# Optimization experiments

Measured on AMD Instinct MI355X. Metric: run time of the kernel, lower is better.

Reference implementation:

```python
import jax, jax.numpy as jnp
import numpy as np

EMBD_SIZE = 128
NUM_HEADS = 8
HEAD_SIZE = 16

def setup_inputs() -> dict:
    key = jax.random.key(0)
    ks = jax.random.split(key, 6)
    B, S = 8, 2048
    x = jax.random.normal(ks[0], (B, S, EMBD_SIZE), dtype=jnp.float32)
    # per-head Linear weights, torch layout [out, in] stacked over heads -> [H, hs, E]
    sc = 1.0 / np.sqrt(EMBD_SIZE)
    Wk = jax.random.normal(ks[1], (NUM_HEADS, HEAD_SIZE, EMBD_SIZE), dtype=jnp.float32) * sc
    Wq = jax.random.normal(ks[2], (NUM_HEADS, HEAD_SIZE, EMBD_SIZE), dtype=jnp.float32) * sc
    Wv = jax.random.normal(ks[3], (NUM_HEADS, HEAD_SIZE, EMBD_SIZE), dtype=jnp.float32) * sc
    Wp = jax.random.normal(ks[4], (EMBD_SIZE, NUM_HEADS * HEAD_SIZE), dtype=jnp.float32) * sc
    bp = jax.random.normal(ks[5], (EMBD_SIZE,), dtype=jnp.float32) * 0.01
    return {"x": x, "Wk": Wk, "Wq": Wq, "Wv": Wv, "Wp": Wp, "bp": bp}

def reference(x, Wk, Wq, Wv, Wp, bp):
    # x: [B,S,E]; W{k,q,v}: [H,hs,E]; Wp: [E,H*hs]
    B, S, E = x.shape
    H, hs, _ = Wk.shape
    q = jnp.einsum('bse,hde->bhsd', x, Wq)
    k = jnp.einsum('bse,hde->bhsd', x, Wk)
    v = jnp.einsum('bse,hde->bhsd', x, Wv)
    # NOTE: original code MULTIPLIES by sqrt(head_size) (k.shape[-1]**0.5)
    scores = jnp.einsum('bhsd,bhtd->bhst', q, k) * (hs ** 0.5)
    wei = jax.nn.softmax(scores, axis=-1)  # dropout is identity in eval mode
    out = jnp.einsum('bhst,bhtd->bhsd', wei, v)
    # concat heads along last dim: [B,S,H*hs]
    out = out.transpose(0, 2, 1, 3).reshape(B, S, H * hs)
    return out @ Wp.T + bp
```

## Files before the change

kernel.cpp:

```cpp
#include <hip/hip_runtime.h>
#include <hip/hip_bf16.h>

constexpr int Bb  = 8;
constexpr int Ss  = 2048;
constexpr int Ee  = 128;
constexpr int Hh  = 8;
constexpr int HSs = 16;
constexpr int QKVSZ = Bb * Hh * Ss * HSs;

typedef _Float16 f16;
typedef __attribute__((ext_vector_type(8)))  _Float16 f16x8;
typedef __attribute__((ext_vector_type(16))) float f32x16;

constexpr float QSCALE = 5.770780163555854f;

__device__ __forceinline__ unsigned pack_rtz(float lo, float hi) {
    union { __fp16 __attribute__((ext_vector_type(2))) h; unsigned u; } c;
    c.h = __builtin_amdgcn_cvt_pkrtz(lo, hi);
    return c.u;
}
__device__ __forceinline__ unsigned pack_rne(float lo, float hi) {
    union { __attribute__((ext_vector_type(2))) _Float16 h; unsigned u; } c;
    c.h[0] = (f16)lo; c.h[1] = (f16)hi;
    return c.u;
}

__global__ __launch_bounds__(256) void prep_w(
    const float* __restrict__ Wq, const float* __restrict__ Wk,
    const float* __restrict__ Wv, const float* __restrict__ Wp,
    f16* __restrict__ wh)
{
    int i = (blockIdx.x * 256 + threadIdx.x) * 4;
    const float* src = (i < 16384) ? (Wq + i)
                     : (i < 32768) ? (Wk + i - 16384)
                     : (i < 49152) ? (Wv + i - 32768) : (Wp + i - 49152);
    float4 v = *(const float4*)src;
    union { f16 h[4]; uint2 u; } c;
    c.h[0] = (f16)v.x; c.h[1] = (f16)v.y; c.h[2] = (f16)v.z; c.h[3] = (f16)v.w;
    *(uint2*)(wh + i) = c.u;
}

__global__ __launch_bounds__(256) void qkv_kernel(
    const float* __restrict__ x, const f16* __restrict__ wh,
    f16* __restrict__ qo, f16* __restrict__ ko, f16* __restrict__ vo)
{
    constexpr int LDW = 136;
    __shared__ __align__(16) f16 Xs[32 * LDW];

    const int mat = blockIdx.y;
    const int rowbase = blockIdx.x * 32;

    for (int idx = threadIdx.x; idx < 32 * 32; idx += 256) {
        const int r = idx >> 5, cp = idx & 31;
        float4 v = *(const float4*)(x + (size_t)(rowbase + r) * Ee + cp * 4);
        union { f16 h[4]; uint2 u; } c;
        c.h[0] = (f16)v.x; c.h[1] = (f16)v.y; c.h[2] = (f16)v.z; c.h[3] = (f16)v.w;
        *(uint2*)&Xs[r * LDW + cp * 4] = c.u;
    }
    __syncthreads();

    const int wv_ = threadIdx.x >> 6, lane = threadIdx.x & 63;
    const int h = lane >> 5, n31 = lane & 31;

    f16x8 A[8];
#pragma unroll
    for (int t = 0; t < 8; ++t)
        A[t] = *(const f16x8*)&Xs[n31 * LDW + 16 * t + 8 * h];

    const int c = wv_ * 32 + n31;
    const f16* wr = wh + mat * 16384 + (size_t)c * Ee + 8 * h;
    f32x16 acc = {};
#pragma unroll
    for (int t = 0; t < 8; ++t)
        acc = __builtin_amdgcn_mfma_f32_32x32x16_f16(A[t], *(const f16x8*)(wr + 16 * t), acc, 0, 0, 0);

    const int b = rowbase >> 11;
    const int s0 = rowbase & 2047;
    const int head = c >> 4, d = c & 15;
    const int bh = b * Hh + head;

    if (mat < 2) {
        f16* dst = (mat == 0) ? qo : ko;
        const float scale = (mat == 1) ? QSCALE : 1.f;
#pragma unroll
        for (int r = 0; r < 16; ++r) {
            const int s = s0 + (r & 3) + 8 * (r >> 2) + 4 * h;
            dst[((size_t)bh * Ss + s) * HSs + d] = (f16)(acc[r] * scale);
        }
    } else {
        const int it = s0 >> 6, g0 = (s0 >> 4) & 3;
        f16* vb = vo + (size_t)bh * 65536 + it * 2048;
#pragma unroll
        for (int rq = 0; rq < 4; ++rq) {
            union { f16 hv[4]; uint2 u; } pk4;
#pragma unroll
            for (int i = 0; i < 4; ++i) pk4.hv[i] = (f16)acc[4 * rq + i];
            *(uint2*)(vb + (g0 + (rq >> 1)) * 512 + (d + 32 * (rq & 1)) * 8 + 4 * h) = pk4.u;
        }
        for (int i = threadIdx.x; i < 512; i += 256) {
            const int gp = i >> 8, hd = (i >> 5) & 7, cc = i & 31;
            const int lanep = (cc < 16) ? 16 + cc : 32 + cc;
            const unsigned one2 = 0x3C003C00u;
            uint4 val = ((cc & 15) == 0) ? (uint4){one2, one2, one2, one2}
                                         : (uint4){0, 0, 0, 0};
            *(uint4*)(vo + (size_t)(b * Hh + hd) * 65536 + it * 2048
                      + (g0 + gp) * 512 + lanep * 8) = val;
        }
    }
}

__device__ __forceinline__ void cb_exchange(const unsigned* pw, int h,
                                            f16x8& Blo, f16x8& Bhi) {
    unsigned exa = (unsigned)__shfl_xor((int)(h ? pw[0] : pw[2]), 32, 64);
    unsigned exb = (unsigned)__shfl_xor((int)(h ? pw[1] : pw[3]), 32, 64);
    unsigned exc = (unsigned)__shfl_xor((int)(h ? pw[4] : pw[6]), 32, 64);
    unsigned exd = (unsigned)__shfl_xor((int)(h ? pw[5] : pw[7]), 32, 64);
    union { unsigned u[4]; f16x8 v; } B1, B2;
    if (h == 0) {
        B1.u[0] = pw[0]; B1.u[1] = pw[1]; B1.u[2] = exa; B1.u[3] = exb;
        B2.u[0] = pw[4]; B2.u[1] = pw[5]; B2.u[2] = exc; B2.u[3] = exd;
    } else {
        B1.u[0] = exa; B1.u[1] = exb; B1.u[2] = pw[2]; B1.u[3] = pw[3];
        B2.u[0] = exc; B2.u[1] = exd; B2.u[2] = pw[6]; B2.u[3] = pw[7];
    }
    Blo = B1.v; Bhi = B2.v;
}

__global__ __launch_bounds__(64, 4) void attn_kernel(
    const f16* __restrict__ qg, const f16* __restrict__ kg,
    const f16* __restrict__ vg, f16* __restrict__ og)
{
    const int blk  = blockIdx.x;
    const int bh   = (blk & 7) * 8 + (blk >> 9);
    const int qblk = (blk >> 3) & 63;
    const int lane = threadIdx.x;
    const int h    = lane >> 5;
    const int q31  = lane & 31;
    const int qbase = qblk * 32;

    const f16x8 qf = *(const f16x8*)(qg + ((size_t)bh * Ss + qbase + q31) * HSs + 8 * h);

    const f16* pk = kg + (size_t)bh * Ss * HSs + q31 * 16 + 8 * h;
    const f16* pv = vg + (size_t)bh * 65536 + lane * 8;

    f16x8 ka0 = *(const f16x8*)pk;
    f16x8 ka1 = *(const f16x8*)(pk + 512);
    f16x8 va0 = *(const f16x8*)(pv);
    f16x8 va1 = *(const f16x8*)(pv + 512);
    f16x8 va2 = *(const f16x8*)(pv + 1024);
    f16x8 va3 = *(const f16x8*)(pv + 1536);

    f32x16 acc = {};
    const f32x16 z16 = {};
    float m = -1e30f;

    for (int it = 0; it < Ss / 64; ++it) {
        f16x8 nk0, nk1, nv0, nv1, nv2, nv3;
        if (it < Ss / 64 - 1) {
            pk += 1024; pv += 2048;
            nk0 = *(const f16x8*)pk;
            nk1 = *(const f16x8*)(pk + 512);
            nv0 = *(const f16x8*)(pv);
            nv1 = *(const f16x8*)(pv + 512);
            nv2 = *(const f16x8*)(pv + 1024);
            nv3 = *(const f16x8*)(pv + 1536);
        }

        f32x16 st0 = __builtin_amdgcn_mfma_f32_32x32x16_f16(ka0, qf, z16, 0, 0, 0);
        f32x16 st1 = __builtin_amdgcn_mfma_f32_32x32x16_f16(ka1, qf, z16, 0, 0, 0);

        float mx = st0[0];
#pragma unroll
        for (int t = 1; t < 16; ++t) mx = fmaxf(mx, st0[t]);
#pragma unroll
        for (int t = 0; t < 16; ++t) mx = fmaxf(mx, st1[t]);
        mx = fmaxf(mx, __shfl_xor(mx, 32, 64));
        const float mnew = fmaxf(m, mx);
        const float corr = __builtin_amdgcn_exp2f(m - mnew);
#pragma unroll
        for (int r = 0; r < 9; ++r) acc[r] *= corr;
        m = mnew;

#pragma unroll
        for (int t = 0; t < 16; ++t) st0[t] = __builtin_amdgcn_exp2f(st0[t] - mnew);
#pragma unroll
        for (int t = 0; t < 16; ++t) st1[t] = __builtin_amdgcn_exp2f(st1[t] - mnew);
        unsigned pw0[8], pw1[8];
#pragma unroll
        for (int r = 0; r < 8; ++r) pw0[r] = pack_rtz(st0[2 * r], st0[2 * r + 1]);
#pragma unroll
        for (int r = 0; r < 8; ++r) pw1[r] = pack_rtz(st1[2 * r], st1[2 * r + 1]);
        f16x8 B1, B2, B3, B4;
        cb_exchange(pw0, h, B1, B2);
        cb_exchange(pw1, h, B3, B4);

        acc = __builtin_amdgcn_mfma_f32_32x32x16_f16(va0, B1, acc, 0, 0, 0);
        acc = __builtin_amdgcn_mfma_f32_32x32x16_f16(va1, B2, acc, 0, 0, 0);
        acc = __builtin_amdgcn_mfma_f32_32x32x16_f16(va2, B3, acc, 0, 0, 0);
        acc = __builtin_amdgcn_mfma_f32_32x32x16_f16(va3, B4, acc, 0, 0, 0);

        ka0 = nk0; ka1 = nk1;
        va0 = nv0; va1 = nv1; va2 = nv2; va3 = nv3;
    }

    const float l = acc[8] + __shfl_xor(acc[8], 32, 64);
    const float inv = 1.f / l;
    const int b = bh >> 3, head = bh & 7;
    f16* op = og + ((size_t)b * Ss + qbase + q31) * Ee + head * HSs;
    uint2 lo = { pack_rne(acc[0] * inv, acc[1] * inv), pack_rne(acc[2] * inv, acc[3] * inv) };
    uint2 hi = { pack_rne(acc[4] * inv, acc[5] * inv), pack_rne(acc[6] * inv, acc[7] * inv) };
    *(uint2*)(op + 4 * h)     = lo;
    *(uint2*)(op + 8 + 4 * h) = hi;
}

__global__ __launch_bounds__(256) void proj_kernel(
    const f16* __restrict__ oh, const f16* __restrict__ wph,
    const float* __restrict__ bp, float* __restrict__ out)
{
    constexpr int LDW = 136;
    __shared__ __align__(16) f16 Os[32 * LDW];
    const int rowbase = blockIdx.x * 32;

    for (int idx = threadIdx.x; idx < 512; idx += 256) {
        const int r = idx >> 4, cp = idx & 15;
        *(f16x8*)&Os[r * LDW + cp * 8] =
            *(const f16x8*)(oh + (size_t)(rowbase + r) * Ee + cp * 8);
    }
    __syncthreads();

    const int wv_ = threadIdx.x >> 6, lane = threadIdx.x & 63;
    const int h = lane >> 5, n31 = lane & 31;

    f16x8 A[8];
#pragma unroll
    for (int t = 0; t < 8; ++t)
        A[t] = *(const f16x8*)&Os[n31 * LDW + 16 * t + 8 * h];

    const int e = wv_ * 32 + n31;
    const f16* wr = wph + (size_t)e * Ee + 8 * h;
    f32x16 acc = {};
#pragma unroll
    for (int t = 0; t < 8; ++t)
        acc = __builtin_amdgcn_mfma_f32_32x32x16_f16(A[t], *(const f16x8*)(wr + 16 * t), acc, 0, 0, 0);

    const float bias = bp[e];
#pragma unroll
    for (int r = 0; r < 16; ++r) {
        const int R = rowbase + (r & 3) + 8 * (r >> 2) + 4 * h;
        out[(size_t)R * Ee + e] = acc[r] + bias;
    }
}

extern "C" void kernel_launch(void* const* d_in, const int* in_sizes, int n_in,
                              void* d_out, int out_size, void* d_ws, size_t ws_size,
                              hipStream_t stream)
{
    const float* x  = (const float*)d_in[0];
    const float* Wk = (const float*)d_in[1];
    const float* Wq = (const float*)d_in[2];
    const float* Wv = (const float*)d_in[3];
    const float* Wp = (const float*)d_in[4];
    const float* bp = (const float*)d_in[5];
    float* out = (float*)d_out;

    f16* ws = (f16*)d_ws;
    f16* qh = ws;
    f16* kh = ws + (size_t)QKVSZ;
    f16* vh = ws + (size_t)2 * QKVSZ;
    f16* oh = ws + (size_t)4 * QKVSZ;
    f16* wh = ws + (size_t)5 * QKVSZ;

    prep_w<<<64, 256, 0, stream>>>(Wq, Wk, Wv, Wp, wh);
    qkv_kernel<<<dim3(Bb * Ss / 32, 3), 256, 0, stream>>>(x, wh, qh, kh, vh);
    attn_kernel<<<Bb * Hh * (Ss / 32), 64, 0, stream>>>(qh, kh, vh, oh);
    proj_kernel<<<Bb * Ss / 32, 256, 0, stream>>>(oh, wh + 49152, bp, out);
}
```

Measured before the change: 136.9 us.

## Fuse QKV projections per block and use lazy softmax rescaling in attention

The QKV kernel now loops over all three weight matrices inside one block, so each x tile is loaded and converted once instead of three times, and the grid drops its y dimension. The attention kernel replaces the per-iteration running-max rescale with a lazy scheme: the max is subtracted and the accumulator corrected only when any score exceeds a threshold, with the offset folded into the MFMA init accumulator. The V layout is changed so the register exchange (cb_exchange shuffles) is no longer needed, and K/V prefetch is split around the MFMAs. The lazy threshold relies on fp16 exp headroom and could overflow or lose precision on unusual score ranges.

```diff
diff --git a/kernel.cpp b/kernel.cpp
--- a/kernel.cpp
+++ b/kernel.cpp
@@ -23,6 +23,17 @@
     union { __attribute__((ext_vector_type(2))) _Float16 h; unsigned u; } c;
     c.h[0] = (f16)lo; c.h[1] = (f16)hi;
     return c.u;
+}
+
+__device__ __forceinline__ float vmax16(const f32x16& v) {
+    float a = fmaxf(fmaxf(v[0],  v[1]),  v[2]);
+    float b = fmaxf(fmaxf(v[3],  v[4]),  v[5]);
+    float c = fmaxf(fmaxf(v[6],  v[7]),  v[8]);
+    float d = fmaxf(fmaxf(v[9],  v[10]), v[11]);
+    float e = fmaxf(fmaxf(v[12], v[13]), v[14]);
+    float g = fmaxf(fmaxf(a, b), c);
+    float h = fmaxf(fmaxf(d, e), v[15]);
+    return fmaxf(g, h);
 }
 
 __global__ __launch_bounds__(256) void prep_w(
@@ -47,15 +58,14 @@
     constexpr int LDW = 136;
     __shared__ __align__(16) f16 Xs[32 * LDW];
 
-    const int mat = blockIdx.y;
     const int rowbase = blockIdx.x * 32;
 
     for (int idx = threadIdx.x; idx < 32 * 32; idx += 256) {
         const int r = idx >> 5, cp = idx & 31;
         float4 v = *(const float4*)(x + (size_t)(rowbase + r) * Ee + cp * 4);
-        union { f16 h[4]; uint2 u; } c;
-        c.h[0] = (f16)v.x; c.h[1] = (f16)v.y; c.h[2] = (f16)v.z; c.h[3] = (f16)v.w;
-        *(uint2*)&Xs[r * LDW + cp * 4] = c.u;
+        union { f16 h[4]; uint2 u; } cv;
+        cv.h[0] = (f16)v.x; cv.h[1] = (f16)v.y; cv.h[2] = (f16)v.z; cv.h[3] = (f16)v.w;
+        *(uint2*)&Xs[r * LDW + cp * 4] = cv.u;
     }
     __syncthreads();
 
@@ -68,62 +78,49 @@
         A[t] = *(const f16x8*)&Xs[n31 * LDW + 16 * t + 8 * h];
 
     const int c = wv_ * 32 + n31;
-    const f16* wr = wh + mat * 16384 + (size_t)c * Ee + 8 * h;
-    f32x16 acc = {};
-#pragma unroll
-    for (int t = 0; t < 8; ++t)
-        acc = __builtin_amdgcn_mfma_f32_32x32x16_f16(A[t], *(const f16x8*)(wr + 16 * t), acc, 0, 0, 0);
-
     const int b = rowbase >> 11;
     const int s0 = rowbase & 2047;
     const int head = c >> 4, d = c & 15;
     const int bh = b * Hh + head;
-
-    if (mat < 2) {
-        f16* dst = (mat == 0) ? qo : ko;
-        const float scale = (mat == 1) ? QSCALE : 1.f;
-#pragma unroll
-        for (int r = 0; r < 16; ++r) {
-            const int s = s0 + (r & 3) + 8 * (r >> 2) + 4 * h;
-            dst[((size_t)bh * Ss + s) * HSs + d] = (f16)(acc[r] * scale);
-        }
-    } else {
-        const int it = s0 >> 6, g0 = (s0 >> 4) & 3;
-        f16* vb = vo + (size_t)bh * 65536 + it * 2048;
-#pragma unroll
-        for (int rq = 0; rq < 4; ++rq) {
-            union { f16 hv[4]; uint2 u; } pk4;
-#pragma unroll
-            for (int i = 0; i < 4; ++i) pk4.hv[i] = (f16)acc[4 * rq + i];
-            *(uint2*)(vb + (g0 + (rq >> 1)) * 512 + (d + 32 * (rq & 1)) * 8 + 4 * h) = pk4.u;
-        }
-        for (int i = threadIdx.x; i < 512; i += 256) {
-            const int gp = i >> 8, hd = (i >> 5) & 7, cc = i & 31;
-            const int lanep = (cc < 16) ? 16 + cc : 32 + cc;
-            const unsigned one2 = 0x3C003C00u;
-            uint4 val = ((cc & 15) == 0) ? (uint4){one2, one2, one2, one2}
-                                         : (uint4){0, 0, 0, 0};
-            *(uint4*)(vo + (size_t)(b * Hh + hd) * 65536 + it * 2048
-                      + (g0 + gp) * 512 + lanep * 8) = val;
-        }
-    }
-}
-
-__device__ __forceinline__ void cb_exchange(const unsigned* pw, int h,
-                                            f16x8& Blo, f16x8& Bhi) {
-    unsigned exa = (unsigned)__shfl_xor((int)(h ? pw[0] : pw[2]), 32, 64);
-    unsigned exb = (unsigned)__shfl_xor((int)(h ? pw[1] : pw[3]), 32, 64);
-    unsigned exc = (unsigned)__shfl_xor((int)(h ? pw[4] : pw[6]), 32, 64);
-    unsigned exd = (unsigned)__shfl_xor((int)(h ? pw[5] : pw[7]), 32, 64);
-    union { unsigned u[4]; f16x8 v; } B1, B2;
-    if (h == 0) {
-        B1.u[0] = pw[0]; B1.u[1] = pw[1]; B1.u[2] = exa; B1.u[3] = exb;
-        B2.u[0] = pw[4]; B2.u[1] = pw[5]; B2.u[2] = exc; B2.u[3] = exd;
-    } else {
-        B1.u[0] = exa; B1.u[1] = exb; B1.u[2] = pw[2]; B1.u[3] = pw[3];
-        B2.u[0] = exc; B2.u[1] = exd; B2.u[2] = pw[6]; B2.u[3] = pw[7];
-    }
-    Blo = B1.v; Bhi = B2.v;
+    const int it = s0 >> 6, g0 = (s0 >> 4) & 3;
+
+#pragma unroll
+    for (int mat = 0; mat < 3; ++mat) {
+        const f16* wr = wh + mat * 16384 + (size_t)c * Ee + 8 * h;
+        f32x16 acc = {};
+#pragma unroll
+        for (int t = 0; t < 8; ++t)
+            acc = __builtin_amdgcn_mfma_f32_32x32x16_f16(A[t], *(const f16x8*)(wr + 16 * t), acc, 0, 0, 0);
+
+        if (mat < 2) {
+            f16* dst = (mat == 0) ? qo : ko;
+            const float scale = (mat == 1) ? QSCALE : 1.f;
+#pragma unroll
+            for (int r = 0; r < 16; ++r) {
+                const int s = s0 + (r & 3) + 8 * (r >> 2) + 4 * h;
+                dst[((size_t)bh * Ss + s) * HSs + d] = (f16)(acc[r] * scale);
+            }
+        } else {
+            f16* vb = vo + (size_t)bh * 65536 + it * 2048;
+#pragma unroll
+            for (int rq = 0; rq < 4; ++rq) {
+                union { f16 hv[4]; uint2 u; } pk4;
+#pragma unroll
+                for (int i = 0; i < 4; ++i) pk4.hv[i] = (f16)acc[4 * rq + i];
+                *(uint2*)(vb + (g0 + (rq >> 1)) * 512 + (d + 32 * h) * 8 + 4 * (rq & 1)) = pk4.u;
+            }
+        }
+    }
+
+    for (int i = threadIdx.x; i < 512; i += 256) {
+        const int gp = i >> 8, hd = (i >> 5) & 7, cc = i & 31;
+        const int lanep = (cc < 16) ? 16 + cc : 32 + cc;
+        const unsigned one2 = 0x3C003C00u;
+        uint4 val = ((cc & 15) == 0) ? (uint4){one2, one2, one2, one2}
+                                     : (uint4){0, 0, 0, 0};
+        *(uint4*)(vo + (size_t)(b * Hh + hd) * 65536 + it * 2048
+                  + (g0 + gp) * 512 + lanep * 8) = val;
+    }
 }
 
 __global__ __launch_bounds__(64, 4) void attn_kernel(
@@ -151,56 +148,58 @@
     f16x8 va3 = *(const f16x8*)(pv + 1536);
 
     f32x16 acc = {};
-    const f32x16 z16 = {};
-    float m = -1e30f;
-
-    for (int it = 0; it < Ss / 64; ++it) {
-        f16x8 nk0, nk1, nv0, nv1, nv2, nv3;
-        if (it < Ss / 64 - 1) {
-            pk += 1024; pv += 2048;
-            nk0 = *(const f16x8*)pk;
-            nk1 = *(const f16x8*)(pk + 512);
-            nv0 = *(const f16x8*)(pv);
-            nv1 = *(const f16x8*)(pv + 512);
-            nv2 = *(const f16x8*)(pv + 1024);
-            nv3 = *(const f16x8*)(pv + 1536);
-        }
-
-        f32x16 st0 = __builtin_amdgcn_mfma_f32_32x32x16_f16(ka0, qf, z16, 0, 0, 0);
-        f32x16 st1 = __builtin_amdgcn_mfma_f32_32x32x16_f16(ka1, qf, z16, 0, 0, 0);
-
-        float mx = st0[0];
-#pragma unroll
-        for (int t = 1; t < 16; ++t) mx = fmaxf(mx, st0[t]);
-#pragma unroll
-        for (int t = 0; t < 16; ++t) mx = fmaxf(mx, st1[t]);
+    f32x16 cinit = {};
+
+    constexpr int NIT = Ss / 64;
+    for (int it = 0; it < NIT; ++it) {
+        f32x16 st0 = __builtin_amdgcn_mfma_f32_32x32x16_f16(ka0, qf, cinit, 0, 0, 0);
+        f32x16 st1 = __builtin_amdgcn_mfma_f32_32x32x16_f16(ka1, qf, cinit, 0, 0, 0);
+
+        if (it + 1 < NIT) {
+            pk += 1024;
+            ka0 = *(const f16x8*)pk;
+            ka1 = *(const f16x8*)(pk + 512);
+        }
+
+        float mx = fmaxf(vmax16(st0), vmax16(st1));
         mx = fmaxf(mx, __shfl_xor(mx, 32, 64));
-        const float mnew = fmaxf(m, mx);
-        const float corr = __builtin_amdgcn_exp2f(m - mnew);
-#pragma unroll
-        for (int r = 0; r < 9; ++r) acc[r] *= corr;
-        m = mnew;
-
-#pragma unroll
-        for (int t = 0; t < 16; ++t) st0[t] = __builtin_amdgcn_exp2f(st0[t] - mnew);
-#pragma unroll
-        for (int t = 0; t < 16; ++t) st1[t] = __builtin_amdgcn_exp2f(st1[t] - mnew);
-        unsigned pw0[8], pw1[8];
-#pragma unroll
-        for (int r = 0; r < 8; ++r) pw0[r] = pack_rtz(st0[2 * r], st0[2 * r + 1]);
-#pragma unroll
-        for (int r = 0; r < 8; ++r) pw1[r] = pack_rtz(st1[2 * r], st1[2 * r + 1]);
-        f16x8 B1, B2, B3, B4;
-        cb_exchange(pw0, h, B1, B2);
-        cb_exchange(pw1, h, B3, B4);
-
-        acc = __builtin_amdgcn_mfma_f32_32x32x16_f16(va0, B1, acc, 0, 0, 0);
-        acc = __builtin_amdgcn_mfma_f32_32x32x16_f16(va1, B2, acc, 0, 0, 0);
-        acc = __builtin_amdgcn_mfma_f32_32x32x16_f16(va2, B3, acc, 0, 0, 0);
-        acc = __builtin_amdgcn_mfma_f32_32x32x16_f16(va3, B4, acc, 0, 0, 0);
-
-        ka0 = nk0; ka1 = nk1;
-        va0 = nv0; va1 = nv1; va2 = nv2; va3 = nv3;
+
+        if (__any(mx > 8.f)) {
+            const float delta = fmaxf(mx, 0.f);
+            const float corr  = __builtin_amdgcn_exp2f(-delta);
+#pragma unroll
+            for (int r = 0; r < 9; ++r) acc[r] *= corr;
+#pragma unroll
+            for (int t = 0; t < 16; ++t) { st0[t] -= delta; st1[t] -= delta; }
+#pragma unroll
+            for (int r = 0; r < 16; ++r) cinit[r] -= delta;
+        }
+
+        union { unsigned u[4]; f16x8 v; } B1, B2, B3, B4;
+#pragma unroll
+        for (int r = 0; r < 4; ++r) {
+            B1.u[r] = pack_rtz(__builtin_amdgcn_exp2f(st0[2 * r]),
+                               __builtin_amdgcn_exp2f(st0[2 * r + 1]));
+            B2.u[r] = pack_rtz(__builtin_amdgcn_exp2f(st0[8 + 2 * r]),
+                               __builtin_amdgcn_exp2f(st0[9 + 2 * r]));
+            B3.u[r] = pack_rtz(__builtin_amdgcn_exp2f(st1[2 * r]),
+                               __builtin_amdgcn_exp2f(st1[2 * r + 1]));
+            B4.u[r] = pack_rtz(__builtin_amdgcn_exp2f(st1[8 + 2 * r]),
+                               __builtin_amdgcn_exp2f(st1[9 + 2 * r]));
+        }
+
+        acc = __builtin_amdgcn_mfma_f32_32x32x16_f16(va0, B1.v, acc, 0, 0, 0);
+        acc = __builtin_amdgcn_mfma_f32_32x32x16_f16(va1, B2.v, acc, 0, 0, 0);
+        acc = __builtin_amdgcn_mfma_f32_32x32x16_f16(va2, B3.v, acc, 0, 0, 0);
+        acc = __builtin_amdgcn_mfma_f32_32x32x16_f16(va3, B4.v, acc, 0, 0, 0);
+
+        if (it + 1 < NIT) {
+            pv += 2048;
+            va0 = *(const f16x8*)(pv);
+            va1 = *(const f16x8*)(pv + 512);
+            va2 = *(const f16x8*)(pv + 1024);
+            va3 = *(const f16x8*)(pv + 1536);
+        }
     }
 
     const float l = acc[8] + __shfl_xor(acc[8], 32, 64);
@@ -271,7 +270,7 @@
     f16* wh = ws + (size_t)5 * QKVSZ;
 
     prep_w<<<64, 256, 0, stream>>>(Wq, Wk, Wv, Wp, wh);
-    qkv_kernel<<<dim3(Bb * Ss / 32, 3), 256, 0, stream>>>(x, wh, qh, kh, vh);
+    qkv_kernel<<<Bb * Ss / 32, 256, 0, stream>>>(x, wh, qh, kh, vh);
     attn_kernel<<<Bb * Hh * (Ss / 32), 64, 0, stream>>>(qh, kh, vh, oh);
     proj_kernel<<<Bb * Ss / 32, 256, 0, stream>>>(oh, wh + 49152, bp, out);
 }
```

Result: no change. 134.3 us (-1.9%).
